# Kernel optimization log

Hardware: AMD Instinct MI355X
Metric: run time of the kernel (lower is better)

## Reference

```python
import jax, jax.numpy as jnp
import numpy as np

STATE_DIM = 1024
INPUT_DIM = 1024
BATCH = 8192


def setup_inputs() -> dict:
    key = jax.random.key(0)
    ks = jax.random.split(key, 7)
    # Kaiming-uniform-ish init like torch Linear
    bx = 1.0 / np.sqrt(INPUT_DIM)
    bh = 1.0 / np.sqrt(STATE_DIM)
    return {
        "x": jax.random.normal(ks[0], (BATCH, INPUT_DIM), jnp.float32),
        "prevh": jax.random.normal(ks[1], (BATCH, STATE_DIM), jnp.float32),
        "prevc": jax.random.normal(ks[2], (BATCH, STATE_DIM), jnp.float32),
        "Wx": jax.random.uniform(ks[3], (INPUT_DIM, 4 * STATE_DIM), jnp.float32, -bx, bx),
        "bx": jax.random.uniform(ks[4], (4 * STATE_DIM,), jnp.float32, -bx, bx),
        "Wh": jax.random.uniform(ks[5], (STATE_DIM, 4 * STATE_DIM), jnp.float32, -bh, bh),
    }


def reference(x, prevh, prevc, Wx, bx, Wh):
    # stacked gate pre-activations: [B, 4*state_dim]
    stacked = x @ Wx + bx + prevh @ Wh
    i_bar, f_bar, o_bar, g_bar = jnp.split(stacked, 4, axis=1)
    i = jax.nn.sigmoid(i_bar)
    f = jax.nn.sigmoid(f_bar)
    o = jax.nn.sigmoid(o_bar)
    g = jnp.tanh(g_bar)
    nextc = prevc * f + g * i
    nexth = jnp.tanh(nextc) * o
    return (nexth, nextc)
```

## Files before the change

### kernel.cpp

```cpp
#include <hip/hip_runtime.h>
#include <hip/hip_bf16.h>


#define BATCH   8192
#define SDIM    1024
#define KDIM    2048
#define NT      32

typedef __attribute__((ext_vector_type(8))) short s16x8;
typedef __attribute__((ext_vector_type(4))) float f32x4;

__device__ __forceinline__ void gload16(const void* g, void* l) {
    __builtin_amdgcn_global_load_lds((const __attribute__((address_space(1))) void*)g,
                                     (__attribute__((address_space(3))) void*)l,
                                     16, 0, 0);
}

__device__ __forceinline__ float fast_sigmoid(float x) {
    return 1.0f / (1.0f + __expf(-x));
}
__device__ __forceinline__ float fast_tanh(float v) {
    float a = fabsf(v);
    float e = __expf(-2.0f * a);
    float t = (1.0f - e) / (1.0f + e);
    return copysignf(t, v);
}

__global__ void convA(const float* __restrict__ x, const float* __restrict__ h,
                      __hip_bfloat16* __restrict__ A) {
    int t = blockIdx.x * blockDim.x + threadIdx.x;
    int e = t << 3;
    int b = e >> 11;
    int k = e & 2047;
    const float* src = (k < 1024) ? (x + (size_t)b * 1024 + k)
                                  : (h + (size_t)b * 1024 + (k - 1024));
    float4 v0 = *(const float4*)(src);
    float4 v1 = *(const float4*)(src + 4);
    union { __hip_bfloat16 b[8]; s16x8 v; } u;
    u.b[0] = __float2bfloat16(v0.x); u.b[1] = __float2bfloat16(v0.y);
    u.b[2] = __float2bfloat16(v0.z); u.b[3] = __float2bfloat16(v0.w);
    u.b[4] = __float2bfloat16(v1.x); u.b[5] = __float2bfloat16(v1.y);
    u.b[6] = __float2bfloat16(v1.z); u.b[7] = __float2bfloat16(v1.w);
    *(s16x8*)(A + e) = u.v;
}

__global__ void convW(const float* __restrict__ Wx, const float* __restrict__ Wh,
                      __hip_bfloat16* __restrict__ Wt) {
    __shared__ float tile[32][33];
    int k0 = blockIdx.x * 32;
    int n0 = blockIdx.y * 32;
    int tx = threadIdx.x;
    int ty = threadIdx.y;
#pragma unroll
    for (int j = 0; j < 4; ++j) {
        int k = k0 + ty + j * 8;
        int n = n0 + tx;
        float v = (k < 1024) ? Wx[(size_t)k * 4096 + n]
                             : Wh[(size_t)(k - 1024) * 4096 + n];
        tile[ty + j * 8][tx] = v;
    }
    __syncthreads();
#pragma unroll
    for (int j = 0; j < 4; ++j) {
        int n = n0 + ty + j * 8;
        int k = k0 + tx;
        int np = ((n & 1023) >> 4) * 64 + (n >> 10) * 16 + (n & 15);
        Wt[(size_t)np * 2048 + k] = __float2bfloat16(tile[tx][ty + j * 8]);
    }
}

__global__ __launch_bounds__(512, 2) void lstm_gemm(
    const __hip_bfloat16* __restrict__ A,
    const __hip_bfloat16* __restrict__ Wt,
    const float* __restrict__ bx,
    const float* __restrict__ prevc,
    float* __restrict__ outh,
    float* __restrict__ outc)
{
    __shared__ __align__(16) char lds[131072];

    const int tid  = threadIdx.x;
    const int lane = tid & 63;
    const int w    = tid >> 6;
    const int wr   = w >> 2;
    const int wc   = w & 3;
    const int l15  = lane & 15;

    const int bid = blockIdx.x;
    const int xcd = bid & 7, j = bid >> 3;
    const int mt = (xcd >> 1) * 8 + (j & 7);
    const int nt = (xcd & 1) * 8 + (j >> 3);
    const int m0 = mt * 256, n0 = nt * 256, S0 = nt * 64;

    const int scol = ((lane & 7) ^ (lane >> 3)) << 3;
    const __hip_bfloat16* Ag = A  + (size_t)m0 * KDIM;
    const __hip_bfloat16* Bg = Wt + (size_t)n0 * KDIM;

    auto SA = [&](int tt, int p) {
        char* dst = lds + (2 * (tt & 1) + p) * 16384 + w * 1024;
        const __hip_bfloat16* src =
            Ag + (size_t)(p * 128 + w * 8 + (lane >> 3)) * KDIM + tt * 64 + scol;
        gload16(src, dst);
        gload16(src + (size_t)64 * KDIM, dst + 8192);
    };
    auto SB = [&](int tt, int p) {
        char* dst = lds + 65536 + (2 * (tt & 1) + p) * 16384 + w * 1024;
        const __hip_bfloat16* src =
            Bg + (size_t)(p * 128 + w * 8 + (lane >> 3)) * KDIM + tt * 64 + scol;
        gload16(src, dst);
        gload16(src + (size_t)64 * KDIM, dst + 8192);
    };

    f32x4 acc[8][4];
#pragma unroll
    for (int m = 0; m < 8; ++m)
#pragma unroll
        for (int g = 0; g < 4; ++g)
            acc[m][g] = (f32x4)0.0f;

    SB(0, 0); SB(0, 1); SA(0, 0); SA(0, 1); SB(1, 0); SB(1, 1);
    asm volatile("s_waitcnt vmcnt(4)" ::: "memory");
    __builtin_amdgcn_s_barrier();

    const int swz0 = (((lane >> 4))     ^ (lane & 7)) << 4;
    const int swz1 = (((lane >> 4) | 4) ^ (lane & 7)) << 4;
    const int brow = (wc & 1) * 64;

    s16x8 af[4][2], bf[4][2];

#define PH_SYNC()                                           \
    __builtin_amdgcn_s_barrier();                           \
    asm volatile("s_waitcnt lgkmcnt(0)" ::: "memory");      \
    __builtin_amdgcn_sched_barrier(0);                      \
    __builtin_amdgcn_s_setprio(1);

#define PH_END()                                            \
    __builtin_amdgcn_s_setprio(0);                          \
    __builtin_amdgcn_s_barrier();

    for (int t = 0; t < NT; ++t) {
        const char* as = lds + (2 * (t & 1) + wr) * 16384;
        const char* bs = lds + 65536 + (2 * (t & 1) + (wc >> 1)) * 16384;

#pragma unroll
        for (int m = 0; m < 4; ++m) {
            af[m][0] = *(const s16x8*)(as + (m * 16 + l15) * 128 + swz0);
            af[m][1] = *(const s16x8*)(as + (m * 16 + l15) * 128 + swz1);
        }
#pragma unroll
        for (int g = 0; g < 2; ++g) {
            bf[g][0] = *(const s16x8*)(bs + (brow + g * 16 + l15) * 128 + swz0);
            bf[g][1] = *(const s16x8*)(bs + (brow + g * 16 + l15) * 128 + swz1);
        }
        if (t + 1 < NT) SA(t + 1, 0);
        PH_SYNC();
#pragma unroll
        for (int m = 0; m < 4; ++m)
#pragma unroll
            for (int g = 0; g < 2; ++g) {
                acc[m][g] = __builtin_amdgcn_mfma_f32_16x16x32_bf16(af[m][0], bf[g][0], acc[m][g], 0, 0, 0);
                acc[m][g] = __builtin_amdgcn_mfma_f32_16x16x32_bf16(af[m][1], bf[g][1], acc[m][g], 0, 0, 0);
            }
        PH_END();

#pragma unroll
        for (int g = 2; g < 4; ++g) {
            bf[g][0] = *(const s16x8*)(bs + (brow + g * 16 + l15) * 128 + swz0);
            bf[g][1] = *(const s16x8*)(bs + (brow + g * 16 + l15) * 128 + swz1);
        }
        if (t + 1 < NT) SA(t + 1, 1);
        PH_SYNC();
#pragma unroll
        for (int m = 0; m < 4; ++m)
#pragma unroll
            for (int g = 2; g < 4; ++g) {
                acc[m][g] = __builtin_amdgcn_mfma_f32_16x16x32_bf16(af[m][0], bf[g][0], acc[m][g], 0, 0, 0);
                acc[m][g] = __builtin_amdgcn_mfma_f32_16x16x32_bf16(af[m][1], bf[g][1], acc[m][g], 0, 0, 0);
            }
        PH_END();

#pragma unroll
        for (int m = 0; m < 4; ++m) {
            af[m][0] = *(const s16x8*)(as + ((m + 4) * 16 + l15) * 128 + swz0);
            af[m][1] = *(const s16x8*)(as + ((m + 4) * 16 + l15) * 128 + swz1);
        }
        if (t + 2 < NT) SB(t + 2, 0);
        PH_SYNC();
#pragma unroll
        for (int m = 0; m < 4; ++m)
#pragma unroll
            for (int g = 2; g < 4; ++g) {
                acc[m + 4][g] = __builtin_amdgcn_mfma_f32_16x16x32_bf16(af[m][0], bf[g][0], acc[m + 4][g], 0, 0, 0);
                acc[m + 4][g] = __builtin_amdgcn_mfma_f32_16x16x32_bf16(af[m][1], bf[g][1], acc[m + 4][g], 0, 0, 0);
            }
        PH_END();

        if (t + 2 < NT) SB(t + 2, 1);
        __builtin_amdgcn_s_barrier();
        __builtin_amdgcn_s_setprio(1);
#pragma unroll
        for (int m = 0; m < 4; ++m)
#pragma unroll
            for (int g = 0; g < 2; ++g) {
                acc[m + 4][g] = __builtin_amdgcn_mfma_f32_16x16x32_bf16(af[m][0], bf[g][0], acc[m + 4][g], 0, 0, 0);
                acc[m + 4][g] = __builtin_amdgcn_mfma_f32_16x16x32_bf16(af[m][1], bf[g][1], acc[m + 4][g], 0, 0, 0);
            }
        __builtin_amdgcn_s_setprio(0);
        if (t + 2 < NT) {
            asm volatile("s_waitcnt vmcnt(4)" ::: "memory");
        } else {
            asm volatile("s_waitcnt vmcnt(0)" ::: "memory");
        }
        __builtin_amdgcn_s_barrier();
    }
#undef PH_SYNC
#undef PH_END

    const int st  = S0 + wc * 16 + l15;
    const float b_i = bx[st];
    const float b_f = bx[1024 + st];
    const float b_o = bx[2048 + st];
    const float b_g = bx[3072 + st];
    const int rbase = m0 + wr * 128 + (lane >> 4) * 4;

#pragma unroll
    for (int m = 0; m < 8; ++m) {
#pragma unroll
        for (int q = 0; q < 4; ++q) {
            int row = rbase + m * 16 + q;
            float ib = acc[m][0][q] + b_i;
            float fb = acc[m][1][q] + b_f;
            float ob = acc[m][2][q] + b_o;
            float gb = acc[m][3][q] + b_g;
            float ig = fast_sigmoid(ib);
            float fg = fast_sigmoid(fb);
            float og = fast_sigmoid(ob);
            float gg = fast_tanh(gb);
            float pc = prevc[(size_t)row * SDIM + st];
            float nc = pc * fg + gg * ig;
            float nh = fast_tanh(nc) * og;
            outh[(size_t)row * SDIM + st] = nh;
            outc[(size_t)row * SDIM + st] = nc;
        }
    }
}

extern "C" void kernel_launch(void* const* d_in, const int* in_sizes, int n_in,
                              void* d_out, int out_size, void* d_ws, size_t ws_size,
                              hipStream_t stream) {
    const float* x     = (const float*)d_in[0];
    const float* prevh = (const float*)d_in[1];
    const float* prevc = (const float*)d_in[2];
    const float* Wx    = (const float*)d_in[3];
    const float* bx    = (const float*)d_in[4];
    const float* Wh    = (const float*)d_in[5];

    __hip_bfloat16* Abf = (__hip_bfloat16*)d_ws;
    __hip_bfloat16* Wt  = Abf + (size_t)BATCH * KDIM;

    float* outh = (float*)d_out;
    float* outc = outh + (size_t)BATCH * SDIM;

    hipLaunchKernelGGL(convA, dim3(8192), dim3(256), 0, stream, x, prevh, Abf);
    hipLaunchKernelGGL(convW, dim3(64, 128), dim3(32, 8), 0, stream, Wx, Wh, Wt);
    hipLaunchKernelGGL(lstm_gemm, dim3(512), dim3(512), 0, stream,
                       Abf, Wt, bx, prevc, outh, outc);
}
```

Measured before the change: 160.7 us.

## Collapse four-phase GEMM main loop into two larger MFMA phases

```diff
diff --git a/kernel.cpp b/kernel.cpp
--- a/kernel.cpp
+++ b/kernel.cpp
@@ -121,6 +121,7 @@
     SB(0, 0); SB(0, 1); SA(0, 0); SA(0, 1); SB(1, 0); SB(1, 1);
     asm volatile("s_waitcnt vmcnt(4)" ::: "memory");
     __builtin_amdgcn_s_barrier();
+    __builtin_amdgcn_sched_barrier(0);
 
     const int swz0 = (((lane >> 4))     ^ (lane & 7)) << 4;
     const int swz1 = (((lane >> 4) | 4) ^ (lane & 7)) << 4;
@@ -128,93 +129,64 @@
 
     s16x8 af[4][2], bf[4][2];
 
-#define PH_SYNC()                                           \
-    __builtin_amdgcn_s_barrier();                           \
-    asm volatile("s_waitcnt lgkmcnt(0)" ::: "memory");      \
-    __builtin_amdgcn_sched_barrier(0);                      \
-    __builtin_amdgcn_s_setprio(1);
-
-#define PH_END()                                            \
-    __builtin_amdgcn_s_setprio(0);                          \
-    __builtin_amdgcn_s_barrier();
-
     for (int t = 0; t < NT; ++t) {
         const char* as = lds + (2 * (t & 1) + wr) * 16384;
         const char* bs = lds + 65536 + (2 * (t & 1) + (wc >> 1)) * 16384;
 
 #pragma unroll
+        for (int g = 0; g < 4; ++g) {
+            bf[g][0] = *(const s16x8*)(bs + (brow + g * 16 + l15) * 128 + swz0);
+            bf[g][1] = *(const s16x8*)(bs + (brow + g * 16 + l15) * 128 + swz1);
+        }
+#pragma unroll
         for (int m = 0; m < 4; ++m) {
             af[m][0] = *(const s16x8*)(as + (m * 16 + l15) * 128 + swz0);
             af[m][1] = *(const s16x8*)(as + (m * 16 + l15) * 128 + swz1);
         }
-#pragma unroll
-        for (int g = 0; g < 2; ++g) {
-            bf[g][0] = *(const s16x8*)(bs + (brow + g * 16 + l15) * 128 + swz0);
-            bf[g][1] = *(const s16x8*)(bs + (brow + g * 16 + l15) * 128 + swz1);
-        }
-        if (t + 1 < NT) SA(t + 1, 0);
-        PH_SYNC();
-#pragma unroll
-        for (int m = 0; m < 4; ++m)
-#pragma unroll
-            for (int g = 0; g < 2; ++g) {
-                acc[m][g] = __builtin_amdgcn_mfma_f32_16x16x32_bf16(af[m][0], bf[g][0], acc[m][g], 0, 0, 0);
-                acc[m][g] = __builtin_amdgcn_mfma_f32_16x16x32_bf16(af[m][1], bf[g][1], acc[m][g], 0, 0, 0);
-            }
-        PH_END();
-
-#pragma unroll
-        for (int g = 2; g < 4; ++g) {
-            bf[g][0] = *(const s16x8*)(bs + (brow + g * 16 + l15) * 128 + swz0);
-            bf[g][1] = *(const s16x8*)(bs + (brow + g * 16 + l15) * 128 + swz1);
-        }
-        if (t + 1 < NT) SA(t + 1, 1);
-        PH_SYNC();
-#pragma unroll
-        for (int m = 0; m < 4; ++m)
-#pragma unroll
-            for (int g = 2; g < 4; ++g) {
-                acc[m][g] = __builtin_amdgcn_mfma_f32_16x16x32_bf16(af[m][0], bf[g][0], acc[m][g], 0, 0, 0);
-                acc[m][g] = __builtin_amdgcn_mfma_f32_16x16x32_bf16(af[m][1], bf[g][1], acc[m][g], 0, 0, 0);
-            }
-        PH_END();
+        if (t + 1 < NT) { SA(t + 1, 0); SA(t + 1, 1); }
+
+        __builtin_amdgcn_s_setprio(1);
+#pragma unroll
+        for (int kf = 0; kf < 2; ++kf)
+#pragma unroll
+            for (int m = 0; m < 4; ++m)
+#pragma unroll
+                for (int g = 0; g < 4; ++g)
+                    acc[m][g] = __builtin_amdgcn_mfma_f32_16x16x32_bf16(
+                        af[m][kf], bf[g][kf], acc[m][g], 0, 0, 0);
+        __builtin_amdgcn_s_setprio(0);
+
+        __builtin_amdgcn_sched_barrier(0);
+        __builtin_amdgcn_s_barrier();
+        __builtin_amdgcn_sched_barrier(0);
 
 #pragma unroll
         for (int m = 0; m < 4; ++m) {
             af[m][0] = *(const s16x8*)(as + ((m + 4) * 16 + l15) * 128 + swz0);
             af[m][1] = *(const s16x8*)(as + ((m + 4) * 16 + l15) * 128 + swz1);
         }
-        if (t + 2 < NT) SB(t + 2, 0);
-        PH_SYNC();
-#pragma unroll
-        for (int m = 0; m < 4; ++m)
-#pragma unroll
-            for (int g = 2; g < 4; ++g) {
-                acc[m + 4][g] = __builtin_amdgcn_mfma_f32_16x16x32_bf16(af[m][0], bf[g][0], acc[m + 4][g], 0, 0, 0);
-                acc[m + 4][g] = __builtin_amdgcn_mfma_f32_16x16x32_bf16(af[m][1], bf[g][1], acc[m + 4][g], 0, 0, 0);
-            }
-        PH_END();
-
-        if (t + 2 < NT) SB(t + 2, 1);
-        __builtin_amdgcn_s_barrier();
+        if (t + 2 < NT) { SB(t + 2, 0); SB(t + 2, 1); }
+
         __builtin_amdgcn_s_setprio(1);
 #pragma unroll
-        for (int m = 0; m < 4; ++m)
-#pragma unroll
-            for (int g = 0; g < 2; ++g) {
-                acc[m + 4][g] = __builtin_amdgcn_mfma_f32_16x16x32_bf16(af[m][0], bf[g][0], acc[m + 4][g], 0, 0, 0);
-                acc[m + 4][g] = __builtin_amdgcn_mfma_f32_16x16x32_bf16(af[m][1], bf[g][1], acc[m + 4][g], 0, 0, 0);
-            }
+        for (int kf = 0; kf < 2; ++kf)
+#pragma unroll
+            for (int m = 0; m < 4; ++m)
+#pragma unroll
+                for (int g = 0; g < 4; ++g)
+                    acc[m + 4][g] = __builtin_amdgcn_mfma_f32_16x16x32_bf16(
+                        af[m][kf], bf[g][kf], acc[m + 4][g], 0, 0, 0);
         __builtin_amdgcn_s_setprio(0);
+
+        __builtin_amdgcn_sched_barrier(0);
         if (t + 2 < NT) {
             asm volatile("s_waitcnt vmcnt(4)" ::: "memory");
         } else {
             asm volatile("s_waitcnt vmcnt(0)" ::: "memory");
         }
         __builtin_amdgcn_s_barrier();
-    }
-#undef PH_SYNC
-#undef PH_END
+        __builtin_amdgcn_sched_barrier(0);
+    }
 
     const int st  = S0 + wc * 16 + l15;
     const float b_i = bx[st];
```

Result: faster. 156.4 us (-2.7%).
